# Performance work log

Hardware: AMD Instinct MI355X
Metric: run time of the kernel (lower is better)

## Reference

```python
import jax, jax.numpy as jnp
import numpy as np

B, C, H, W = 4, 256, 64, 64

def _conv1x1(x, Wt, b):
    # x: [b,c,h,w], Wt: [out,in], b: [out]
    return jnp.einsum('bchw,dc->bdhw', x, Wt) + b[None, :, None, None]

def setup_inputs() -> dict:
    key = jax.random.key(0)
    ks = jax.random.split(key, 10)
    s = 1.0 / np.sqrt(C)
    return {
        'F_c': jax.random.normal(ks[0], (B, C, H, W), jnp.float32),
        'F_s': jax.random.normal(ks[1], (B, C, H, W), jnp.float32),
        'Wf': jax.random.normal(ks[2], (C, C), jnp.float32) * s,
        'bf': jnp.zeros((C,), jnp.float32),
        'Wg': jax.random.normal(ks[3], (C, C), jnp.float32) * s,
        'bg': jnp.zeros((C,), jnp.float32),
        'Wh': jax.random.normal(ks[4], (C, C), jnp.float32) * s,
        'bh': jnp.zeros((C,), jnp.float32),
        'Wo': jax.random.normal(ks[5], (C, C), jnp.float32) * s,
        'bo': jnp.zeros((C,), jnp.float32),
    }

def reference(F_c, F_s, Wf, bf, Wg, bg, Wh, bh, Wo, bo):
    b, c, h, w = F_c.shape
    Fq = _conv1x1(F_c, Wf, bf).reshape(b, c, -1)          # [b,c,Nc]
    G = _conv1x1(F_s, Wg, bg).reshape(b, c, -1)           # [b,c,Ns]
    Hv = _conv1x1(F_s, Wh, bh).reshape(b, c, -1)          # [b,c,Ns]
    S = jnp.einsum('bcn,bcm->bnm', Fq, G)                 # [b,Nc,Ns] (unscaled)
    S = jax.nn.softmax(S, axis=-1)
    res = jnp.einsum('bcm,bnm->bcn', Hv, S)               # [b,c,Nc]
    res = res.reshape(b, c, h, w)
    return _conv1x1(res, Wo, bo)
```

## Files before the change

### kernel.cpp

```cpp
#include <hip/hip_runtime.h>
#include <stdint.h>

#define NB 4
#define CC 256
#define NN 4096
#define KITERS 32
#define WAIT_LGKM0 0xC07F

typedef __attribute__((ext_vector_type(8))) _Float16 half8;
typedef __attribute__((ext_vector_type(4))) _Float16 half4;
typedef __attribute__((ext_vector_type(2))) _Float16 half2v;
typedef __attribute__((ext_vector_type(4))) float floatx4;
typedef __attribute__((ext_vector_type(16))) float float16v;
typedef __attribute__((ext_vector_type(4))) int intx4;

__device__ __forceinline__ void cvt16(const float4* src, half8& lo, half8& hi) {
  float4 a = src[0], b = src[1], c = src[2], d = src[3];
  lo[0] = (_Float16)a.x; lo[1] = (_Float16)a.y; lo[2] = (_Float16)a.z; lo[3] = (_Float16)a.w;
  lo[4] = (_Float16)b.x; lo[5] = (_Float16)b.y; lo[6] = (_Float16)b.z; lo[7] = (_Float16)b.w;
  hi[0] = (_Float16)c.x; hi[1] = (_Float16)c.y; hi[2] = (_Float16)c.z; hi[3] = (_Float16)c.w;
  hi[4] = (_Float16)d.x; hi[5] = (_Float16)d.y; hi[6] = (_Float16)d.z; hi[7] = (_Float16)d.w;
}

__global__ __launch_bounds__(256) void k_transpose(const float* __restrict__ Fc,
                                                   const float* __restrict__ Fs,
                                                   _Float16* __restrict__ Xct,
                                                   _Float16* __restrict__ Xst) {
  __shared__ float t[64][65];
  const int nt = blockIdx.x, ct = blockIdx.y, bz = blockIdx.z;
  const int b = bz >> 1;
  const float* src = ((bz & 1) ? Fs : Fc) + (size_t)b * CC * NN;
  _Float16* dst = ((bz & 1) ? Xst : Xct) + (size_t)b * NN * CC;
  const int tid = threadIdx.x;
  const int n0 = nt * 64, c0 = ct * 64;
  const int col = tid & 63, row4 = tid >> 6;
#pragma unroll
  for (int i = 0; i < 16; i++) {
    int c = row4 + i * 4;
    t[c][col] = src[(size_t)(c0 + c) * NN + n0 + col];
  }
  __syncthreads();
#pragma unroll
  for (int i = 0; i < 16; i++) {
    int n = row4 + i * 4;
    dst[(size_t)(n0 + n) * CC + c0 + col] = (_Float16)t[col][n];
  }
}

__global__ __launch_bounds__(256, 2) void k_qkv(const float* __restrict__ Wf,
                                                const float* __restrict__ Wg,
                                                const float* __restrict__ Wh,
                                                const _Float16* __restrict__ Xct,
                                                const _Float16* __restrict__ Xst,
                                                const float* __restrict__ bf,
                                                const float* __restrict__ bg,
                                                const float* __restrict__ bh,
                                                _Float16* __restrict__ Qs,
                                                _Float16* __restrict__ Ks,
                                                _Float16* __restrict__ Vs) {
  __shared__ _Float16 As[128][40];
  __shared__ _Float16 Bs[128][40];
  const int z = blockIdx.z, bz = blockIdx.y;
  const float* W = (z == 0) ? Wf : ((z == 1) ? Wg : Wh);
  const _Float16* X = ((z == 0) ? Xct : Xst) + (size_t)bz * NN * CC;
  const float* bias = (z == 0) ? bf : ((z == 1) ? bg : bh);
  int mt, nt;
  if (z < 2) { mt = blockIdx.x >> 5; nt = blockIdx.x & 31; }
  else       { mt = blockIdx.x >> 1; nt = blockIdx.x & 1;  }
  const int m0 = mt * 128, n0 = nt * 128;
  const int tid = threadIdx.x;
  const int wave = tid >> 6, lane = tid & 63, quad = lane >> 4, l15 = lane & 15;
  const int wm = (wave >> 1) * 64, wn = (wave & 1) * 64;

  floatx4 acc[4][4];
#pragma unroll
  for (int i = 0; i < 4; i++)
#pragma unroll
    for (int j = 0; j < 4; j++) acc[i][j] = (floatx4){0.f, 0.f, 0.f, 0.f};

  const int srow = tid >> 1;
  const int shalf = (tid & 1) * 16;

  for (int kk = 0; kk < 256; kk += 32) {
    half8 a_lo, a_hi, b_lo, b_hi;
    if (z < 2) {
      cvt16((const float4*)(W + (size_t)(m0 + srow) * 256 + kk + shalf), a_lo, a_hi);
      const _Float16* bp = X + (size_t)(n0 + srow) * 256 + kk + shalf;
      b_lo = *(const half8*)bp; b_hi = *(const half8*)(bp + 8);
    } else {
      const _Float16* ap = X + (size_t)(m0 + srow) * 256 + kk + shalf;
      a_lo = *(const half8*)ap; a_hi = *(const half8*)(ap + 8);
      cvt16((const float4*)(W + (size_t)(n0 + srow) * 256 + kk + shalf), b_lo, b_hi);
    }
    __syncthreads();
    *(half8*)&As[srow][shalf] = a_lo;
    *(half8*)&As[srow][shalf + 8] = a_hi;
    *(half8*)&Bs[srow][shalf] = b_lo;
    *(half8*)&Bs[srow][shalf + 8] = b_hi;
    __syncthreads();
    half8 af[4], bfr[4];
#pragma unroll
    for (int mb = 0; mb < 4; mb++) af[mb] = *(const half8*)&As[wm + mb * 16 + l15][quad * 8];
#pragma unroll
    for (int nb = 0; nb < 4; nb++) bfr[nb] = *(const half8*)&Bs[wn + nb * 16 + l15][quad * 8];
#pragma unroll
    for (int mb = 0; mb < 4; mb++)
#pragma unroll
      for (int nb = 0; nb < 4; nb++)
        acc[mb][nb] = __builtin_amdgcn_mfma_f32_16x16x32_f16(af[mb], bfr[nb], acc[mb][nb], 0, 0, 0);
  }

  if (z < 2) {
    _Float16* op = (z == 0 ? Qs : Ks) + (size_t)bz * NN * CC;
#pragma unroll
    for (int mb = 0; mb < 4; mb++) {
      int d0 = m0 + wm + mb * 16 + quad * 4;
      float b0 = bias[d0], b1 = bias[d0 + 1], b2 = bias[d0 + 2], b3 = bias[d0 + 3];
      const int cs = d0 >> 4, hh = (d0 >> 3) & 1, j0 = d0 & 7;
#pragma unroll
      for (int nb = 0; nb < 4; nb++) {
        int n_ = n0 + wn + nb * 16 + l15;
        int kt = n_ >> 5, ql_ = n_ & 31;
        half4 pk;
        pk[0] = (_Float16)(acc[mb][nb][0] + b0);
        pk[1] = (_Float16)(acc[mb][nb][1] + b1);
        pk[2] = (_Float16)(acc[mb][nb][2] + b2);
        pk[3] = (_Float16)(acc[mb][nb][3] + b3);
        size_t idx = ((size_t)(kt * 16 + cs) * 64 + ql_ + 32 * hh) * 8 + j0;
        *(half4*)(op + idx) = pk;
      }
    }
  } else {
    _Float16* op = Vs + (size_t)bz * NN * CC;
#pragma unroll
    for (int mb = 0; mb < 4; mb++) {
      int nq0 = m0 + wm + mb * 16 + quad * 4;
      const int kt = nq0 >> 5, krel = nq0 & 31;
      const int hk = krel >> 4, hh = (krel >> 3) & 1, j0 = krel & 7;
#pragma unroll
      for (int nb = 0; nb < 4; nb++) {
        int d = n0 + wn + nb * 16 + l15;
        int ql_ = d & 31, g = (d >> 5) & 7;
        float bv = bias[d];
        half4 pk;
        pk[0] = (_Float16)(acc[mb][nb][0] + bv);
        pk[1] = (_Float16)(acc[mb][nb][1] + bv);
        pk[2] = (_Float16)(acc[mb][nb][2] + bv);
        pk[3] = (_Float16)(acc[mb][nb][3] + bv);
        size_t idx = (((size_t)(kt * 8 + g) * 2 + hk) * 64 + ql_ + 32 * hh) * 8 + j0;
        *(half4*)(op + idx) = pk;
      }
    }
  }
}

__global__ __launch_bounds__(256, 2) void k_attn(const _Float16* __restrict__ Q,
                                                 const _Float16* __restrict__ K,
                                                 const _Float16* __restrict__ Vt,
                                                 _Float16* __restrict__ Opart,
                                                 float2* __restrict__ Ml) {
  __shared__ _Float16 smem[8192 * 3 + 4096];
  const int tid = threadIdx.x;
  const int wave = tid >> 6, lane = tid & 63;
  _Float16* Kl = smem;
  _Float16* Plw = smem + 3 * 8192 + wave * 1024;

  const int qt = blockIdx.x, ck = blockIdx.y, b = blockIdx.z;
  const int ql = lane & 31, h = lane >> 5;
  const int q0 = qt * 128 + wave * 32;
  const _Float16* Qb = Q + (size_t)b * NN * CC;
  const _Float16* Kb = K + (size_t)b * NN * CC;
  const _Float16* Vb = Vt + (size_t)b * NN * CC;
  const int kt_base = ck * (1024 / 32);

  const int ktq = q0 >> 5;
  half8 qf[16];
#pragma unroll
  for (int cs = 0; cs < 16; cs++)
    qf[cs] = *(const half8*)(Qb + ((size_t)(ktq * 16 + cs) * 64 + lane) * 8);

  float16v Oa[8];
#pragma unroll
  for (int g = 0; g < 8; g++)
#pragma unroll
    for (int i = 0; i < 16; i++) Oa[g][i] = 0.f;

  float m_run = -1e30f, l_run = 0.f;

  intx4 kpre[4], vpre[4];
  {
    const _Float16* Kt = Kb + (size_t)kt_base * 8192;
    const _Float16* Vtile = Vb + (size_t)kt_base * 8192;
#pragma unroll
    for (int p = 0; p < 4; p++) {
      kpre[p] = *(const intx4*)(Kt + tid * 8 + p * 2048);
      vpre[p] = *(const intx4*)(Vtile + tid * 8 + p * 2048);
    }
  }

  for (int t = 0; t < KITERS; t++) {
    const int vb = t & 1;
    _Float16* Vw = smem + (1 + vb) * 8192;
    __syncthreads();
#pragma unroll
    for (int p = 0; p < 4; p++) {
      *(intx4*)(Kl + tid * 8 + p * 2048) = kpre[p];
      *(intx4*)(Vw + tid * 8 + p * 2048) = vpre[p];
    }
    __syncthreads();
    if (t + 1 < KITERS) {
      const _Float16* Kt = Kb + (size_t)(kt_base + t + 1) * 8192;
      const _Float16* Vtile = Vb + (size_t)(kt_base + t + 1) * 8192;
#pragma unroll
      for (int p = 0; p < 4; p++) {
        kpre[p] = *(const intx4*)(Kt + tid * 8 + p * 2048);
        vpre[p] = *(const intx4*)(Vtile + tid * 8 + p * 2048);
      }
    }

    float16v s;
#pragma unroll
    for (int i = 0; i < 16; i++) s[i] = 0.f;
    if (t > 0) {
      _Float16* Vr = smem + (1 + (vb ^ 1)) * 8192;
      half8 pf0 = *(const half8*)(Plw + lane * 8);
      half8 pf1 = *(const half8*)(Plw + 512 + lane * 8);
#pragma unroll
      for (int u = 0; u < 8; u++) {
        half8 kfa = *(const half8*)(Kl + (2 * u) * 512 + lane * 8);
        s = __builtin_amdgcn_mfma_f32_32x32x16_f16(kfa, qf[2 * u], s, 0, 0, 0);
        half8 vfa = *(const half8*)(Vr + (u * 2) * 512 + lane * 8);
        Oa[u] = __builtin_amdgcn_mfma_f32_32x32x16_f16(vfa, pf0, Oa[u], 0, 0, 0);
        half8 kfb = *(const half8*)(Kl + (2 * u + 1) * 512 + lane * 8);
        s = __builtin_amdgcn_mfma_f32_32x32x16_f16(kfb, qf[2 * u + 1], s, 0, 0, 0);
        half8 vfb = *(const half8*)(Vr + (u * 2 + 1) * 512 + lane * 8);
        Oa[u] = __builtin_amdgcn_mfma_f32_32x32x16_f16(vfb, pf1, Oa[u], 0, 0, 0);
      }
    } else {
#pragma unroll
      for (int cs = 0; cs < 16; cs++) {
        half8 kf = *(const half8*)(Kl + cs * 512 + lane * 8);
        s = __builtin_amdgcn_mfma_f32_32x32x16_f16(kf, qf[cs], s, 0, 0, 0);
      }
    }

    float t0 = fmaxf(s[0], s[1]), t1 = fmaxf(s[2], s[3]);
    float t2 = fmaxf(s[4], s[5]), t3 = fmaxf(s[6], s[7]);
    float t4 = fmaxf(s[8], s[9]), t5 = fmaxf(s[10], s[11]);
    float t6 = fmaxf(s[12], s[13]), t7 = fmaxf(s[14], s[15]);
    t0 = fmaxf(t0, t1); t2 = fmaxf(t2, t3); t4 = fmaxf(t4, t5); t6 = fmaxf(t6, t7);
    float tmax = fmaxf(fmaxf(t0, t2), fmaxf(t4, t6));
    tmax = fmaxf(tmax, __shfl_xor(tmax, 32));
    bool need = tmax > m_run + 8.0f;
    if (__any((int)need)) {
      float mN = need ? tmax : m_run;
      float alpha = __expf(m_run - mN);
      m_run = mN;
      l_run *= alpha;
#pragma unroll
      for (int g = 0; g < 8; g++)
#pragma unroll
        for (int i = 0; i < 16; i++) Oa[g][i] *= alpha;
    }
#pragma unroll
    for (int i = 0; i < 16; i++) s[i] = __expf(s[i] - m_run);
    float u0 = (s[0] + s[1]) + (s[2] + s[3]);
    float u1 = (s[4] + s[5]) + (s[6] + s[7]);
    float u2 = (s[8] + s[9]) + (s[10] + s[11]);
    float u3 = (s[12] + s[13]) + (s[14] + s[15]);
    float ts = (u0 + u1) + (u2 + u3);
    ts += __shfl_xor(ts, 32);
    l_run += ts;
#pragma unroll
    for (int r = 0; r < 16; r += 2) {
      half2v pk;
      pk[0] = (_Float16)s[r];
      pk[1] = (_Float16)s[r + 1];
      int k = (r & 3) + 8 * (r >> 2) + 4 * h;
      *(half2v*)(Plw + (k >> 4) * 512 + (ql + 32 * ((k >> 3) & 1)) * 8 + (k & 7)) = pk;
    }
  }

  {
    _Float16* Vr = smem + (1 + ((KITERS - 1) & 1)) * 8192;
    half8 pf0 = *(const half8*)(Plw + lane * 8);
    half8 pf1 = *(const half8*)(Plw + 512 + lane * 8);
#pragma unroll
    for (int u = 0; u < 8; u++) {
      half8 vfa = *(const half8*)(Vr + (u * 2) * 512 + lane * 8);
      Oa[u] = __builtin_amdgcn_mfma_f32_32x32x16_f16(vfa, pf0, Oa[u], 0, 0, 0);
      half8 vfb = *(const half8*)(Vr + (u * 2 + 1) * 512 + lane * 8);
      Oa[u] = __builtin_amdgcn_mfma_f32_32x32x16_f16(vfb, pf1, Oa[u], 0, 0, 0);
    }
  }

  float invl = 1.f / l_run;
  __syncthreads();
  float* ot = (float*)smem + wave * (32 * 33);
  _Float16* Opb = Opart + ((size_t)ck * NB + b) * NN * CC;
  const int qr = lane >> 1;
  const int chalf = (lane & 1) * 16;
#pragma unroll
  for (int g = 0; g < 8; g++) {
#pragma unroll
    for (int r = 0; r < 16; r++)
      ot[((r & 3) + 8 * (r >> 2) + 4 * h) * 33 + ql] = Oa[g][r] * invl;
    __builtin_amdgcn_s_waitcnt(WAIT_LGKM0);
    half8 o0, o1;
#pragma unroll
    for (int i = 0; i < 8; i++) o0[i] = (_Float16)ot[(chalf + i) * 33 + qr];
#pragma unroll
    for (int i = 0; i < 8; i++) o1[i] = (_Float16)ot[(chalf + 8 + i) * 33 + qr];
    _Float16* gp = Opb + (size_t)(q0 + qr) * CC + g * 32 + chalf;
    *(half8*)gp = o0;
    *(half8*)(gp + 8) = o1;
    __builtin_amdgcn_s_waitcnt(WAIT_LGKM0);
  }
  if (h == 0) {
    float2 ml; ml.x = m_run; ml.y = l_run;
    Ml[((size_t)ck * NB + b) * NN + q0 + ql] = ml;
  }
}

__global__ __launch_bounds__(256, 2) void k_out(const _Float16* __restrict__ Opart,
                                                const float2* __restrict__ Ml,
                                                const float* __restrict__ Wo,
                                                const float* __restrict__ bo,
                                                float* __restrict__ out) {
  __shared__ _Float16 As[128][40];
  __shared__ _Float16 Bs[128][40];
  const int bz = blockIdx.y;
  const int mt = blockIdx.x >> 1, nt = blockIdx.x & 1;
  const int m0 = mt * 128, n0 = nt * 128;
  const int tid = threadIdx.x;
  const int wave = tid >> 6, lane = tid & 63, quad = lane >> 4, l15 = lane & 15;
  const int wm = (wave >> 1) * 64, wn = (wave & 1) * 64;

  floatx4 acc[4][4];
#pragma unroll
  for (int i = 0; i < 4; i++)
#pragma unroll
    for (int j = 0; j < 4; j++) acc[i][j] = (floatx4){0.f, 0.f, 0.f, 0.f};

  const int srow = tid >> 1;
  const int shalf = (tid & 1) * 16;

  const size_t qi = (size_t)bz * NN + m0 + srow;
  float2 a0 = Ml[qi], a1 = Ml[(size_t)NB * NN + qi];
  float2 a2 = Ml[(size_t)2 * NB * NN + qi], a3 = Ml[(size_t)3 * NB * NN + qi];
  float M = fmaxf(fmaxf(a0.x, a1.x), fmaxf(a2.x, a3.x));
  float w0 = __expf(a0.x - M) * a0.y, w1 = __expf(a1.x - M) * a1.y;
  float w2 = __expf(a2.x - M) * a2.y, w3 = __expf(a3.x - M) * a3.y;
  float inv = 1.f / (w0 + w1 + w2 + w3);
  w0 *= inv; w1 *= inv; w2 *= inv; w3 *= inv;
  const size_t ps = (size_t)NB * NN * CC;
  const _Float16* prow = Opart + qi * CC;

  for (int kk = 0; kk < 256; kk += 32) {
    const _Float16* pr = prow + kk + shalf;
    half8 p0a = *(const half8*)pr,            p0b = *(const half8*)(pr + 8);
    half8 p1a = *(const half8*)(pr + ps),     p1b = *(const half8*)(pr + ps + 8);
    half8 p2a = *(const half8*)(pr + 2 * ps), p2b = *(const half8*)(pr + 2 * ps + 8);
    half8 p3a = *(const half8*)(pr + 3 * ps), p3b = *(const half8*)(pr + 3 * ps + 8);
    half8 ma, mb2;
#pragma unroll
    for (int i = 0; i < 8; i++) {
      ma[i] = (_Float16)(w0 * (float)p0a[i] + w1 * (float)p1a[i] +
                         w2 * (float)p2a[i] + w3 * (float)p3a[i]);
      mb2[i] = (_Float16)(w0 * (float)p0b[i] + w1 * (float)p1b[i] +
                          w2 * (float)p2b[i] + w3 * (float)p3b[i]);
    }
    half8 b_lo, b_hi;
    cvt16((const float4*)(Wo + (size_t)(n0 + srow) * 256 + kk + shalf), b_lo, b_hi);
    __syncthreads();
    *(half8*)&As[srow][shalf] = ma;
    *(half8*)&As[srow][shalf + 8] = mb2;
    *(half8*)&Bs[srow][shalf] = b_lo;
    *(half8*)&Bs[srow][shalf + 8] = b_hi;
    __syncthreads();
    half8 af[4], bfr[4];
#pragma unroll
    for (int mb = 0; mb < 4; mb++) af[mb] = *(const half8*)&As[wm + mb * 16 + l15][quad * 8];
#pragma unroll
    for (int nb = 0; nb < 4; nb++) bfr[nb] = *(const half8*)&Bs[wn + nb * 16 + l15][quad * 8];
#pragma unroll
    for (int mb = 0; mb < 4; mb++)
#pragma unroll
      for (int nb = 0; nb < 4; nb++)
        acc[mb][nb] = __builtin_amdgcn_mfma_f32_16x16x32_f16(af[mb], bfr[nb], acc[mb][nb], 0, 0, 0);
  }

  float* op = out + (size_t)bz * NN * CC;
#pragma unroll
  for (int mb = 0; mb < 4; mb++) {
    int nq0 = m0 + wm + mb * 16 + quad * 4;
#pragma unroll
    for (int nb = 0; nb < 4; nb++) {
      int d = n0 + wn + nb * 16 + l15;
      float bv = bo[d];
      floatx4 pk;
      pk[0] = acc[mb][nb][0] + bv;
      pk[1] = acc[mb][nb][1] + bv;
      pk[2] = acc[mb][nb][2] + bv;
      pk[3] = acc[mb][nb][3] + bv;
      *(floatx4*)(op + (size_t)d * NN + nq0) = pk;
    }
  }
}

extern "C" void kernel_launch(void* const* d_in, const int* in_sizes, int n_in,
                              void* d_out, int out_size, void* d_ws, size_t ws_size,
                              hipStream_t stream) {
  const float* Fc = (const float*)d_in[0];
  const float* Fs = (const float*)d_in[1];
  const float* Wf = (const float*)d_in[2];
  const float* bf_ = (const float*)d_in[3];
  const float* Wg = (const float*)d_in[4];
  const float* bg = (const float*)d_in[5];
  const float* Wh = (const float*)d_in[6];
  const float* bh = (const float*)d_in[7];
  const float* Wo = (const float*)d_in[8];
  const float* bo = (const float*)d_in[9];

  char* ws = (char*)d_ws;
  const size_t sz = (size_t)NB * NN * CC * sizeof(_Float16);
  _Float16* Xct = (_Float16*)(ws + 0 * sz);
  _Float16* Xst = (_Float16*)(ws + 1 * sz);
  _Float16* Opart = Xct;
  _Float16* Qs = (_Float16*)(ws + 4 * sz);
  _Float16* Ks = (_Float16*)(ws + 5 * sz);
  _Float16* Vs = (_Float16*)(ws + 6 * sz);
  float2* Ml = (float2*)(ws + 7 * sz);

  k_transpose<<<dim3(64, 4, 8), 256, 0, stream>>>(Fc, Fs, Xct, Xst);
  k_qkv<<<dim3(64, NB, 3), 256, 0, stream>>>(Wf, Wg, Wh, Xct, Xst, bf_, bg, bh, Qs, Ks, Vs);
  k_attn<<<dim3(32, 4, NB), 256, 0, stream>>>(Qs, Ks, Vs, Opart, Ml);
  k_out<<<dim3(64, NB), 256, 0, stream>>>(Opart, Ml, Wo, bo, (float*)d_out);
}
```

Before: 216.5 us.

## Fuse input transpose into QKV projection and split score accumulators

Removes the separate transpose kernel. The QKV GEMM now reads the fp32 NCHW inputs directly, transposes them through a shared-memory staging tile and converts them to fp16 on the fly. Global loads for the next k-step are register-prefetched, and the launch-bounds occupancy hint rises to 3. The attention kernel splits the QK^T MFMA chain into two independent accumulators to shorten the dependency chain. The fused path costs more shared memory and an extra barrier per k-step, and the F and Fs inputs are now reread by every block that uses them.

```diff
diff --git a/kernel.cpp b/kernel.cpp
--- a/kernel.cpp
+++ b/kernel.cpp
@@ -14,60 +14,38 @@
 typedef __attribute__((ext_vector_type(16))) float float16v;
 typedef __attribute__((ext_vector_type(4))) int intx4;
 
-__device__ __forceinline__ void cvt16(const float4* src, half8& lo, half8& hi) {
-  float4 a = src[0], b = src[1], c = src[2], d = src[3];
+__device__ __forceinline__ void cvt16v(float4 a, float4 b, float4 c, float4 d,
+                                       half8& lo, half8& hi) {
   lo[0] = (_Float16)a.x; lo[1] = (_Float16)a.y; lo[2] = (_Float16)a.z; lo[3] = (_Float16)a.w;
   lo[4] = (_Float16)b.x; lo[5] = (_Float16)b.y; lo[6] = (_Float16)b.z; lo[7] = (_Float16)b.w;
   hi[0] = (_Float16)c.x; hi[1] = (_Float16)c.y; hi[2] = (_Float16)c.z; hi[3] = (_Float16)c.w;
   hi[4] = (_Float16)d.x; hi[5] = (_Float16)d.y; hi[6] = (_Float16)d.z; hi[7] = (_Float16)d.w;
 }
 
-__global__ __launch_bounds__(256) void k_transpose(const float* __restrict__ Fc,
-                                                   const float* __restrict__ Fs,
-                                                   _Float16* __restrict__ Xct,
-                                                   _Float16* __restrict__ Xst) {
-  __shared__ float t[64][65];
-  const int nt = blockIdx.x, ct = blockIdx.y, bz = blockIdx.z;
-  const int b = bz >> 1;
-  const float* src = ((bz & 1) ? Fs : Fc) + (size_t)b * CC * NN;
-  _Float16* dst = ((bz & 1) ? Xst : Xct) + (size_t)b * NN * CC;
-  const int tid = threadIdx.x;
-  const int n0 = nt * 64, c0 = ct * 64;
-  const int col = tid & 63, row4 = tid >> 6;
-#pragma unroll
-  for (int i = 0; i < 16; i++) {
-    int c = row4 + i * 4;
-    t[c][col] = src[(size_t)(c0 + c) * NN + n0 + col];
-  }
-  __syncthreads();
-#pragma unroll
-  for (int i = 0; i < 16; i++) {
-    int n = row4 + i * 4;
-    dst[(size_t)(n0 + n) * CC + c0 + col] = (_Float16)t[col][n];
-  }
-}
-
-__global__ __launch_bounds__(256, 2) void k_qkv(const float* __restrict__ Wf,
+__global__ __launch_bounds__(256, 3) void k_qkv(const float* __restrict__ Fc,
+                                                const float* __restrict__ Fs,
+                                                const float* __restrict__ Wf,
                                                 const float* __restrict__ Wg,
                                                 const float* __restrict__ Wh,
-                                                const _Float16* __restrict__ Xct,
-                                                const _Float16* __restrict__ Xst,
                                                 const float* __restrict__ bf,
                                                 const float* __restrict__ bg,
                                                 const float* __restrict__ bh,
                                                 _Float16* __restrict__ Qs,
                                                 _Float16* __restrict__ Ks,
                                                 _Float16* __restrict__ Vs) {
+  __shared__ float tmp[32][132];
   __shared__ _Float16 As[128][40];
   __shared__ _Float16 Bs[128][40];
   const int z = blockIdx.z, bz = blockIdx.y;
+  const float* F = ((z == 0) ? Fc : Fs) + (size_t)bz * CC * NN;
   const float* W = (z == 0) ? Wf : ((z == 1) ? Wg : Wh);
-  const _Float16* X = ((z == 0) ? Xct : Xst) + (size_t)bz * NN * CC;
   const float* bias = (z == 0) ? bf : ((z == 1) ? bg : bh);
   int mt, nt;
   if (z < 2) { mt = blockIdx.x >> 5; nt = blockIdx.x & 31; }
   else       { mt = blockIdx.x >> 1; nt = blockIdx.x & 1;  }
   const int m0 = mt * 128, n0 = nt * 128;
+  const int xn0 = (z < 2) ? n0 : m0;
+  const int wd0 = (z < 2) ? m0 : n0;
   const int tid = threadIdx.x;
   const int wave = tid >> 6, lane = tid & 63, quad = lane >> 4, l15 = lane & 15;
   const int wm = (wave >> 1) * 64, wn = (wave & 1) * 64;
@@ -78,25 +56,52 @@
 #pragma unroll
     for (int j = 0; j < 4; j++) acc[i][j] = (floatx4){0.f, 0.f, 0.f, 0.f};
 
-  const int srow = tid >> 1;
-  const int shalf = (tid & 1) * 16;
+  const int srow = tid >> 1, shalf = (tid & 1) * 16;
+  const int fc = tid >> 3, fn = (tid & 7) * 16;
+  const int xr = tid >> 1, xh = (tid & 1) * 16;
+
+  float4 wr0, wr1, wr2, wr3, fr0, fr1, fr2, fr3;
+  {
+    const float4* wp = (const float4*)(W + (size_t)(wd0 + srow) * 256 + 0 + shalf);
+    wr0 = wp[0]; wr1 = wp[1]; wr2 = wp[2]; wr3 = wp[3];
+    const float4* fp = (const float4*)(F + (size_t)(0 + fc) * NN + xn0 + fn);
+    fr0 = fp[0]; fr1 = fp[1]; fr2 = fp[2]; fr3 = fp[3];
+  }
 
   for (int kk = 0; kk < 256; kk += 32) {
-    half8 a_lo, a_hi, b_lo, b_hi;
+    __syncthreads();
+    *(float4*)&tmp[fc][fn + 0] = fr0;
+    *(float4*)&tmp[fc][fn + 4] = fr1;
+    *(float4*)&tmp[fc][fn + 8] = fr2;
+    *(float4*)&tmp[fc][fn + 12] = fr3;
+    half8 w_lo, w_hi;
+    cvt16v(wr0, wr1, wr2, wr3, w_lo, w_hi);
     if (z < 2) {
-      cvt16((const float4*)(W + (size_t)(m0 + srow) * 256 + kk + shalf), a_lo, a_hi);
-      const _Float16* bp = X + (size_t)(n0 + srow) * 256 + kk + shalf;
-      b_lo = *(const half8*)bp; b_hi = *(const half8*)(bp + 8);
+      *(half8*)&As[srow][shalf] = w_lo;
+      *(half8*)&As[srow][shalf + 8] = w_hi;
     } else {
-      const _Float16* ap = X + (size_t)(m0 + srow) * 256 + kk + shalf;
-      a_lo = *(const half8*)ap; a_hi = *(const half8*)(ap + 8);
-      cvt16((const float4*)(W + (size_t)(n0 + srow) * 256 + kk + shalf), b_lo, b_hi);
-    }
-    __syncthreads();
-    *(half8*)&As[srow][shalf] = a_lo;
-    *(half8*)&As[srow][shalf + 8] = a_hi;
-    *(half8*)&Bs[srow][shalf] = b_lo;
-    *(half8*)&Bs[srow][shalf + 8] = b_hi;
+      *(half8*)&Bs[srow][shalf] = w_lo;
+      *(half8*)&Bs[srow][shalf + 8] = w_hi;
+    }
+    __syncthreads();
+    if (kk + 32 < 256) {
+      const float4* wp = (const float4*)(W + (size_t)(wd0 + srow) * 256 + kk + 32 + shalf);
+      wr0 = wp[0]; wr1 = wp[1]; wr2 = wp[2]; wr3 = wp[3];
+      const float4* fp = (const float4*)(F + (size_t)(kk + 32 + fc) * NN + xn0 + fn);
+      fr0 = fp[0]; fr1 = fp[1]; fr2 = fp[2]; fr3 = fp[3];
+    }
+    half8 xlo, xhi;
+#pragma unroll
+    for (int i = 0; i < 8; i++) xlo[i] = (_Float16)tmp[xh + i][xr];
+#pragma unroll
+    for (int i = 0; i < 8; i++) xhi[i] = (_Float16)tmp[xh + 8 + i][xr];
+    if (z < 2) {
+      *(half8*)&Bs[xr][xh] = xlo;
+      *(half8*)&Bs[xr][xh + 8] = xhi;
+    } else {
+      *(half8*)&As[xr][xh] = xlo;
+      *(half8*)&As[xr][xh + 8] = xhi;
+    }
     __syncthreads();
     half8 af[4], bfr[4];
 #pragma unroll
@@ -218,9 +223,9 @@
       }
     }
 
-    float16v s;
-#pragma unroll
-    for (int i = 0; i < 16; i++) s[i] = 0.f;
+    float16v s, s2;
+#pragma unroll
+    for (int i = 0; i < 16; i++) { s[i] = 0.f; s2[i] = 0.f; }
     if (t > 0) {
       _Float16* Vr = smem + (1 + (vb ^ 1)) * 8192;
       half8 pf0 = *(const half8*)(Plw + lane * 8);
@@ -232,17 +237,21 @@
         half8 vfa = *(const half8*)(Vr + (u * 2) * 512 + lane * 8);
         Oa[u] = __builtin_amdgcn_mfma_f32_32x32x16_f16(vfa, pf0, Oa[u], 0, 0, 0);
         half8 kfb = *(const half8*)(Kl + (2 * u + 1) * 512 + lane * 8);
-        s = __builtin_amdgcn_mfma_f32_32x32x16_f16(kfb, qf[2 * u + 1], s, 0, 0, 0);
+        s2 = __builtin_amdgcn_mfma_f32_32x32x16_f16(kfb, qf[2 * u + 1], s2, 0, 0, 0);
         half8 vfb = *(const half8*)(Vr + (u * 2 + 1) * 512 + lane * 8);
         Oa[u] = __builtin_amdgcn_mfma_f32_32x32x16_f16(vfb, pf1, Oa[u], 0, 0, 0);
       }
     } else {
 #pragma unroll
-      for (int cs = 0; cs < 16; cs++) {
-        half8 kf = *(const half8*)(Kl + cs * 512 + lane * 8);
-        s = __builtin_amdgcn_mfma_f32_32x32x16_f16(kf, qf[cs], s, 0, 0, 0);
+      for (int cs = 0; cs < 16; cs += 2) {
+        half8 kfa = *(const half8*)(Kl + cs * 512 + lane * 8);
+        s = __builtin_amdgcn_mfma_f32_32x32x16_f16(kfa, qf[cs], s, 0, 0, 0);
+        half8 kfb = *(const half8*)(Kl + (cs + 1) * 512 + lane * 8);
+        s2 = __builtin_amdgcn_mfma_f32_32x32x16_f16(kfb, qf[cs + 1], s2, 0, 0, 0);
       }
     }
+#pragma unroll
+    for (int i = 0; i < 16; i++) s[i] += s2[i];
 
     float t0 = fmaxf(s[0], s[1]), t1 = fmaxf(s[2], s[3]);
     float t2 = fmaxf(s[4], s[5]), t3 = fmaxf(s[6], s[7]);
@@ -370,8 +379,9 @@
       mb2[i] = (_Float16)(w0 * (float)p0b[i] + w1 * (float)p1b[i] +
                           w2 * (float)p2b[i] + w3 * (float)p3b[i]);
     }
+    const float4* wp = (const float4*)(Wo + (size_t)(n0 + srow) * 256 + kk + shalf);
     half8 b_lo, b_hi;
-    cvt16((const float4*)(Wo + (size_t)(n0 + srow) * 256 + kk + shalf), b_lo, b_hi);
+    cvt16v(wp[0], wp[1], wp[2], wp[3], b_lo, b_hi);
     __syncthreads();
     *(half8*)&As[srow][shalf] = ma;
     *(half8*)&As[srow][shalf + 8] = mb2;
@@ -424,16 +434,13 @@
 
   char* ws = (char*)d_ws;
   const size_t sz = (size_t)NB * NN * CC * sizeof(_Float16);
-  _Float16* Xct = (_Float16*)(ws + 0 * sz);
-  _Float16* Xst = (_Float16*)(ws + 1 * sz);
-  _Float16* Opart = Xct;
+  _Float16* Opart = (_Float16*)(ws + 0 * sz);
   _Float16* Qs = (_Float16*)(ws + 4 * sz);
   _Float16* Ks = (_Float16*)(ws + 5 * sz);
   _Float16* Vs = (_Float16*)(ws + 6 * sz);
   float2* Ml = (float2*)(ws + 7 * sz);
 
-  k_transpose<<<dim3(64, 4, 8), 256, 0, stream>>>(Fc, Fs, Xct, Xst);
-  k_qkv<<<dim3(64, NB, 3), 256, 0, stream>>>(Wf, Wg, Wh, Xct, Xst, bf_, bg, bh, Qs, Ks, Vs);
+  k_qkv<<<dim3(64, NB, 3), 256, 0, stream>>>(Fc, Fs, Wf, Wg, Wh, bf_, bg, bh, Qs, Ks, Vs);
   k_attn<<<dim3(32, 4, NB), 256, 0, stream>>>(Qs, Ks, Vs, Opart, Ml);
   k_out<<<dim3(64, NB), 256, 0, stream>>>(Opart, Ml, Wo, bo, (float*)d_out);
 }
```

Result: faster. 212.1 us (-2.1%).
